# Kernel tuning notes

Hardware: AMD Instinct MI355X
Metric: run time of the kernel (lower is better)

Reference implementation:

```python
import jax, jax.numpy as jnp
import numpy as np

SCALE = 1.0  # module scale
# dropout is treated as identity (eval mode / deterministic reference)

def setup_inputs() -> dict:
    key = jax.random.key(0)
    k_x, k_w, k1, k2, k3 = jax.random.split(key, 5)
    B, S, D = 4, 4096, 1280
    x = jax.random.normal(k_x, (B, S, D), dtype=jnp.float32)
    W = jax.random.normal(k_w, (D, D), dtype=jnp.float32) * 0.02  # linear.weight [out, in]
    # kron factors are initialized to identity in the module; perturb slightly
    # so the rotation is non-trivial for correctness testing.
    kron_1 = jnp.eye(4, dtype=jnp.float32) + 0.01 * jax.random.normal(k1, (4, 4), dtype=jnp.float32)
    kron_2 = jnp.eye(8, dtype=jnp.float32) + 0.01 * jax.random.normal(k2, (8, 8), dtype=jnp.float32)
    kron_3 = jnp.eye(40, dtype=jnp.float32) + 0.01 * jax.random.normal(k3, (40, 40), dtype=jnp.float32)
    return {"x": x, "W": W, "kron_1": kron_1, "kron_2": kron_2, "kron_3": kron_3}

def reference(x, W, kron_1, kron_2, kron_3):
    # rotate_matrix = kron(kron(k1, k2), k3)  -> [in, in] = [1280, 1280]
    R = jnp.kron(jnp.kron(kron_1, kron_2), kron_3)
    # rotated_weight = (R @ W^T)^T ; F.linear(x, rotated_weight) = x @ (R @ W^T)
    rotated_weight = (R @ W.T).T  # [out, in]
    out = jnp.einsum('bsd,od->bso', x, rotated_weight)
    return out * SCALE
```

## Files before the change

kernel.cpp:

```cpp
#include <hip/hip_runtime.h>
#include <hip/hip_bf16.h>
#include <stdint.h>

typedef __bf16 bf16x8 __attribute__((ext_vector_type(8)));
typedef float floatx4 __attribute__((ext_vector_type(4)));

__device__ __forceinline__ void async_copy16(void* lds, const void* g) {
    __builtin_amdgcn_global_load_lds(
        (const __attribute__((address_space(1))) unsigned int*)g,
        (__attribute__((address_space(3))) unsigned int*)lds,
        16, 0, 0);
}

__global__ __launch_bounds__(256)
void prep(const float* __restrict__ x,
          const float* __restrict__ W,
          const float* __restrict__ K1,
          const float* __restrict__ K2,
          const float* __restrict__ K3,
          __hip_bfloat16* __restrict__ x_bf,
          __hip_bfloat16* __restrict__ Wrot,
          int nConv) {
    const int tid = threadIdx.x;

    if ((int)blockIdx.x < nConv) {
        const size_t i = ((size_t)blockIdx.x * 256 + tid) * 8;
        const float4 a = *(const float4*)(x + i);
        const float4 b = *(const float4*)(x + i + 4);
        bf16x8 v;
        v[0] = (__bf16)a.x; v[1] = (__bf16)a.y; v[2] = (__bf16)a.z; v[3] = (__bf16)a.w;
        v[4] = (__bf16)b.x; v[5] = (__bf16)b.y; v[6] = (__bf16)b.z; v[7] = (__bf16)b.w;
        *(bf16x8*)((__bf16*)x_bf + i) = v;
        return;
    }

    const int o = blockIdx.x - nConv;
    __shared__ __align__(16) float w0[1280];
    __shared__ __align__(16) float t1[1280];
    __shared__ __align__(16) float k3s[1600];
    __shared__ float k2s[64];
    __shared__ float k1s[16];

    for (int i = tid; i < 1280; i += 256) w0[i] = W[o * 1280 + i];
    for (int i = tid; i < 1600; i += 256) k3s[i] = K3[i];
    if (tid < 64) k2s[tid] = K2[tid];
    if (tid < 16) k1s[tid] = K1[tid];
    __syncthreads();

    for (int i = tid; i < 1280; i += 256) {
        const int p = i / 40, d3 = i % 40;
        const float4* w4 = (const float4*)(w0 + p * 40);
        const float4* k4 = (const float4*)(k3s + d3 * 40);
        float acc = 0.f;
#pragma unroll
        for (int t = 0; t < 10; ++t) {
            const float4 a = w4[t], b = k4[t];
            acc += a.x * b.x + a.y * b.y + a.z * b.z + a.w * b.w;
        }
        t1[i] = acc;
    }
    __syncthreads();

    for (int i = tid; i < 1280; i += 256) {
        const int d3 = i % 40, pd = i / 40;
        const int k1 = pd >> 3, d2 = pd & 7;
        float acc = 0.f;
#pragma unroll
        for (int k2 = 0; k2 < 8; ++k2) acc += t1[(k1 * 8 + k2) * 40 + d3] * k2s[d2 * 8 + k2];
        w0[i] = acc;
    }
    __syncthreads();

    for (int i = tid; i < 1280; i += 256) {
        const int d3 = i % 40, pd = i / 40;
        const int d1 = pd >> 3, d2 = pd & 7;
        float acc = 0.f;
#pragma unroll
        for (int k1 = 0; k1 < 4; ++k1) acc += w0[(k1 * 8 + d2) * 40 + d3] * k1s[d1 * 4 + k1];
        Wrot[(size_t)o * 1280 + i] = __float2bfloat16(acc);
    }
}

#define BM 128
#define BN 128
#define BK 64

__global__ __launch_bounds__(256)
void gemm_bt(const __hip_bfloat16* __restrict__ A,
             const __hip_bfloat16* __restrict__ B,
             float* __restrict__ C,
             int M, int N, int K) {
    __shared__ bf16x8 As[1024];
    __shared__ bf16x8 Bs[1024];

    const int tid  = threadIdx.x;
    const int wave = tid >> 6;
    const int lane = tid & 63;
    const int q    = lane >> 4;
    const int r16  = lane & 15;

    const int nTilesN = N / BN;
    const int nTilesM = M / BM;
    const int chunk   = nTilesM >> 3;
    const int xcd = blockIdx.x & 7;
    const int s   = blockIdx.x >> 3;
    const int bm  = xcd * chunk + s / nTilesN;
    const int bn  = s % nTilesN;
    const int tileM = bm * BM, tileN = bn * BN;
    const int wm = wave >> 1, wn = wave & 1;

    floatx4 acc[4][4];
#pragma unroll
    for (int i = 0; i < 4; ++i)
#pragma unroll
        for (int j = 0; j < 4; ++j) acc[i][j] = (floatx4){0.f, 0.f, 0.f, 0.f};

    for (int kt = 0; kt < K; kt += BK) {
#pragma unroll
        for (int t = 0; t < 4; ++t) {
            const int g  = wave * 256 + t * 64 + lane;
            const int m  = g >> 3;
            const int kv = (g & 7) ^ (m & 7);
            async_copy16(&As[wave * 256 + t * 64],
                         A + (size_t)(tileM + m) * K + kt + kv * 8);
            async_copy16(&Bs[wave * 256 + t * 64],
                         B + (size_t)(tileN + m) * K + kt + kv * 8);
        }
        __syncthreads();

#pragma unroll
        for (int s2 = 0; s2 < 2; ++s2) {
            bf16x8 af[4], bfr[4];
            const int kv = s2 * 4 + q;
#pragma unroll
            for (int i = 0; i < 4; ++i) {
                const int m = wm * 64 + i * 16 + r16;
                af[i] = As[m * 8 + (kv ^ (m & 7))];
                const int n = wn * 64 + i * 16 + r16;
                bfr[i] = Bs[n * 8 + (kv ^ (n & 7))];
            }
#pragma unroll
            for (int i = 0; i < 4; ++i)
#pragma unroll
                for (int j = 0; j < 4; ++j)
                    acc[i][j] = __builtin_amdgcn_mfma_f32_16x16x32_bf16(
                        af[i], bfr[j], acc[i][j], 0, 0, 0);
        }
        __syncthreads();
    }

#pragma unroll
    for (int i = 0; i < 4; ++i) {
#pragma unroll
        for (int j = 0; j < 4; ++j) {
            const int col = tileN + wn * 64 + j * 16 + r16;
#pragma unroll
            for (int r = 0; r < 4; ++r) {
                const int row = tileM + wm * 64 + i * 16 + q * 4 + r;
                C[(size_t)row * N + col] = acc[i][j][r];
            }
        }
    }
}

extern "C" void kernel_launch(void* const* d_in, const int* in_sizes, int n_in,
                              void* d_out, int out_size, void* d_ws, size_t ws_size,
                              hipStream_t stream) {
    const float* x  = (const float*)d_in[0];
    const float* W  = (const float*)d_in[1];
    const float* K1 = (const float*)d_in[2];
    const float* K2 = (const float*)d_in[3];
    const float* K3 = (const float*)d_in[4];
    float* out = (float*)d_out;

    const int D = 1280;
    const int M = in_sizes[0] / D;
    const int N = D, K = D;

    __hip_bfloat16* x_bf = (__hip_bfloat16*)d_ws;
    __hip_bfloat16* Wrot = x_bf + (size_t)M * K;

    const int nConv = (M * K) / (256 * 8);
    prep<<<nConv + D, 256, 0, stream>>>(x, W, K1, K2, K3, x_bf, Wrot, nConv);
    gemm_bt<<<(M / BM) * (N / BN), 256, 0, stream>>>(x_bf, Wrot, out, M, N, K);
}
```

Baseline: 240.1 us.

## Triple-buffer GEMM LDS tiles with async prefetch and a 256x128 block tile

The bf16 GEMM now uses a 256x128 output tile with 512 threads (8 waves). Global-to-LDS copies are triple-buffered, with tiles prefetched two k-steps ahead. Explicit vmcnt waits and raw barriers replace the per-step load-then-sync pattern, and the MFMA sections raise wave priority. The aim is to hide global load latency behind matrix math and cut barrier stalls. The cost is about 147KB of LDS per block, so only one block fits per CU despite the launch bound asking for two.

New measurement: 252.8 us. 5.3% more time.

```diff
diff --git a/kernel.cpp b/kernel.cpp
--- a/kernel.cpp
+++ b/kernel.cpp
@@ -81,17 +81,42 @@
     }
 }
 
-#define BM 128
+#define BM 256
 #define BN 128
 #define BK 64
-
-__global__ __launch_bounds__(256)
+#define AG (BM * BK / 8)
+#define BG (BN * BK / 8)
+
+__device__ __forceinline__ void stage_tile(const __hip_bfloat16* __restrict__ A,
+                                           const __hip_bfloat16* __restrict__ B,
+                                           bf16x8* Asb, bf16x8* Bsb,
+                                           int tileM, int tileN, int K, int kt,
+                                           int wave, int lane) {
+#pragma unroll
+    for (int c = 0; c < 4; ++c) {
+        const int g  = c * 512 + wave * 64 + lane;
+        const int m  = g >> 3;
+        const int kv = (g & 7) ^ (m & 7);
+        async_copy16(&Asb[c * 512 + wave * 64],
+                     A + (size_t)(tileM + m) * K + kt + kv * 8);
+    }
+#pragma unroll
+    for (int c = 0; c < 2; ++c) {
+        const int g  = c * 512 + wave * 64 + lane;
+        const int m  = g >> 3;
+        const int kv = (g & 7) ^ (m & 7);
+        async_copy16(&Bsb[c * 512 + wave * 64],
+                     B + (size_t)(tileN + m) * K + kt + kv * 8);
+    }
+}
+
+__global__ __launch_bounds__(512, 2)
 void gemm_bt(const __hip_bfloat16* __restrict__ A,
              const __hip_bfloat16* __restrict__ B,
              float* __restrict__ C,
              int M, int N, int K) {
-    __shared__ bf16x8 As[1024];
-    __shared__ bf16x8 Bs[1024];
+    __shared__ bf16x8 As[3 * AG];
+    __shared__ bf16x8 Bs[3 * BG];
 
     const int tid  = threadIdx.x;
     const int wave = tid >> 6;
@@ -115,19 +140,29 @@
 #pragma unroll
         for (int j = 0; j < 4; ++j) acc[i][j] = (floatx4){0.f, 0.f, 0.f, 0.f};
 
-    for (int kt = 0; kt < K; kt += BK) {
-#pragma unroll
-        for (int t = 0; t < 4; ++t) {
-            const int g  = wave * 256 + t * 64 + lane;
-            const int m  = g >> 3;
-            const int kv = (g & 7) ^ (m & 7);
-            async_copy16(&As[wave * 256 + t * 64],
-                         A + (size_t)(tileM + m) * K + kt + kv * 8);
-            async_copy16(&Bs[wave * 256 + t * 64],
-                         B + (size_t)(tileN + m) * K + kt + kv * 8);
-        }
-        __syncthreads();
-
+    const int nk = K / BK;
+
+    stage_tile(A, B, &As[0], &Bs[0], tileM, tileN, K, 0, wave, lane);
+    if (nk > 1)
+        stage_tile(A, B, &As[AG], &Bs[BG], tileM, tileN, K, BK, wave, lane);
+
+    int cur = 0;
+    for (int t = 0; t < nk; ++t) {
+        if (t + 2 < nk) {
+            const int nx = (cur >= 1) ? cur - 1 : cur + 2;
+            stage_tile(A, B, &As[nx * AG], &Bs[nx * BG],
+                       tileM, tileN, K, (t + 2) * BK, wave, lane);
+            asm volatile("s_waitcnt vmcnt(12)" ::: "memory");
+        } else if (t + 1 < nk) {
+            asm volatile("s_waitcnt vmcnt(6)" ::: "memory");
+        } else {
+            asm volatile("s_waitcnt vmcnt(0)" ::: "memory");
+        }
+        __builtin_amdgcn_s_barrier();
+        asm volatile("" ::: "memory");
+
+        const bf16x8* Ab = &As[cur * AG];
+        const bf16x8* Bb = &Bs[cur * BG];
 #pragma unroll
         for (int s2 = 0; s2 < 2; ++s2) {
             bf16x8 af[4], bfr[4];
@@ -135,18 +170,22 @@
 #pragma unroll
             for (int i = 0; i < 4; ++i) {
                 const int m = wm * 64 + i * 16 + r16;
-                af[i] = As[m * 8 + (kv ^ (m & 7))];
+                af[i] = Ab[m * 8 + (kv ^ (m & 7))];
                 const int n = wn * 64 + i * 16 + r16;
-                bfr[i] = Bs[n * 8 + (kv ^ (n & 7))];
+                bfr[i] = Bb[n * 8 + (kv ^ (n & 7))];
             }
+            __builtin_amdgcn_s_setprio(1);
 #pragma unroll
             for (int i = 0; i < 4; ++i)
 #pragma unroll
                 for (int j = 0; j < 4; ++j)
                     acc[i][j] = __builtin_amdgcn_mfma_f32_16x16x32_bf16(
                         af[i], bfr[j], acc[i][j], 0, 0, 0);
-        }
-        __syncthreads();
+            __builtin_amdgcn_s_setprio(0);
+        }
+        asm volatile("" ::: "memory");
+        __builtin_amdgcn_s_barrier();
+        cur = (cur == 2) ? 0 : cur + 1;
     }
 
 #pragma unroll
@@ -182,5 +221,5 @@
 
     const int nConv = (M * K) / (256 * 8);
     prep<<<nConv + D, 256, 0, stream>>>(x, W, K1, K2, K3, x_bf, Wrot, nConv);
-    gemm_bt<<<(M / BM) * (N / BN), 256, 0, stream>>>(x_bf, Wrot, out, M, N, K);
-}
+    gemm_bt<<<(M / BM) * (N / BN), 512, 0, stream>>>(x_bf, Wrot, out, M, N, K);
+}
```

## Restructure GEMM into 256x320 tiles with double-buffered LDS and interleaved prefetch

Applied to the files above, without the earlier changes.

The GEMM moves to 512-thread blocks computing 256x320 output tiles, so 1280 columns split into four N-tiles and the grid becomes 64x4 = 256 blocks. LDS is double-buffered, and the next K-slice's async global-to-LDS loads are spread across four MFMA phases with explicit waitcnt, barriers, sched_barrier and setprio, so copies overlap compute instead of stalling on a full sync each iteration. Larger tiles also raise operand reuse. The cost is 160 fp32 accumulators per thread and more LDS, which lowers occupancy. The hand-placed vmcnt values and block-wide barriers are fragile if the load counts change.

Result: faster. 219.1 us (-8.7%).

```diff
diff --git a/kernel.cpp b/kernel.cpp
--- a/kernel.cpp
+++ b/kernel.cpp
@@ -81,82 +81,190 @@
     }
 }
 
-#define BM 128
-#define BN 128
+#define BM 256
+#define BN 320
 #define BK 64
-
-__global__ __launch_bounds__(256)
+#define AGRAN 2048
+#define BGRAN 2560
+
+__global__ __launch_bounds__(512, 2)
 void gemm_bt(const __hip_bfloat16* __restrict__ A,
              const __hip_bfloat16* __restrict__ B,
              float* __restrict__ C,
              int M, int N, int K) {
-    __shared__ bf16x8 As[1024];
-    __shared__ bf16x8 Bs[1024];
+    __shared__ bf16x8 As[2][AGRAN];
+    __shared__ bf16x8 Bs[2][BGRAN];
 
     const int tid  = threadIdx.x;
     const int wave = tid >> 6;
     const int lane = tid & 63;
     const int q    = lane >> 4;
     const int r16  = lane & 15;
+    const int wm   = wave >> 2;
+    const int wn   = wave & 3;
 
     const int nTilesN = N / BN;
-    const int nTilesM = M / BM;
-    const int chunk   = nTilesM >> 3;
+    const int chunkM  = (M / BM) >> 3;
     const int xcd = blockIdx.x & 7;
     const int s   = blockIdx.x >> 3;
-    const int bm  = xcd * chunk + s / nTilesN;
+    const int bm  = xcd * chunkM + s / nTilesN;
     const int bn  = s % nTilesN;
     const int tileM = bm * BM, tileN = bn * BN;
-    const int wm = wave >> 1, wn = wave & 1;
-
-    floatx4 acc[4][4];
-#pragma unroll
-    for (int i = 0; i < 4; ++i)
-#pragma unroll
-        for (int j = 0; j < 4; ++j) acc[i][j] = (floatx4){0.f, 0.f, 0.f, 0.f};
-
-    for (int kt = 0; kt < K; kt += BK) {
-#pragma unroll
-        for (int t = 0; t < 4; ++t) {
-            const int g  = wave * 256 + t * 64 + lane;
-            const int m  = g >> 3;
-            const int kv = (g & 7) ^ (m & 7);
-            async_copy16(&As[wave * 256 + t * 64],
-                         A + (size_t)(tileM + m) * K + kt + kv * 8);
-            async_copy16(&Bs[wave * 256 + t * 64],
-                         B + (size_t)(tileN + m) * K + kt + kv * 8);
-        }
-        __syncthreads();
-
-#pragma unroll
-        for (int s2 = 0; s2 < 2; ++s2) {
-            bf16x8 af[4], bfr[4];
-            const int kv = s2 * 4 + q;
-#pragma unroll
-            for (int i = 0; i < 4; ++i) {
-                const int m = wm * 64 + i * 16 + r16;
-                af[i] = As[m * 8 + (kv ^ (m & 7))];
-                const int n = wn * 64 + i * 16 + r16;
-                bfr[i] = Bs[n * 8 + (kv ^ (n & 7))];
-            }
-#pragma unroll
-            for (int i = 0; i < 4; ++i)
-#pragma unroll
-                for (int j = 0; j < 4; ++j)
-                    acc[i][j] = __builtin_amdgcn_mfma_f32_16x16x32_bf16(
-                        af[i], bfr[j], acc[i][j], 0, 0, 0);
-        }
-        __syncthreads();
-    }
-
-#pragma unroll
-    for (int i = 0; i < 4; ++i) {
-#pragma unroll
-        for (int j = 0; j < 4; ++j) {
-            const int col = tileN + wn * 64 + j * 16 + r16;
+
+    uint32_t aoff[4], boff[5];
+#pragma unroll
+    for (int c = 0; c < 4; ++c) {
+        const int g = c * 512 + tid;
+        const int m = g >> 3, kv = (g & 7) ^ (m & 7);
+        aoff[c] = (uint32_t)(((tileM + m) * K + kv * 8) * 2);
+    }
+#pragma unroll
+    for (int c = 0; c < 5; ++c) {
+        const int g = c * 512 + tid;
+        const int m = g >> 3, kv = (g & 7) ^ (m & 7);
+        boff[c] = (uint32_t)(((tileN + m) * K + kv * 8) * 2);
+    }
+    const char* Abase = (const char*)A;
+    const char* Bbase = (const char*)B;
+
+    int ai[8], bi[5];
+#pragma unroll
+    for (int i = 0; i < 8; ++i) {
+        const int m = wm * 128 + i * 16 + r16;
+        ai[i] = m * 8 + (q ^ (m & 7));
+    }
+#pragma unroll
+    for (int j = 0; j < 5; ++j) {
+        const int n = wn * 80 + j * 16 + r16;
+        bi[j] = n * 8 + (q ^ (n & 7));
+    }
+
+    floatx4 acc[8][5];
+#pragma unroll
+    for (int i = 0; i < 8; ++i)
+#pragma unroll
+        for (int j = 0; j < 5; ++j) acc[i][j] = (floatx4){0.f, 0.f, 0.f, 0.f};
+
+    const int nk = K / BK;
+
+#pragma unroll
+    for (int c = 0; c < 4; ++c)
+        async_copy16(&As[0][c * 512 + wave * 64], Abase + aoff[c]);
+#pragma unroll
+    for (int c = 0; c < 5; ++c)
+        async_copy16(&Bs[0][c * 512 + wave * 64], Bbase + boff[c]);
+    asm volatile("s_waitcnt vmcnt(0)" ::: "memory");
+    __builtin_amdgcn_s_barrier();
+
+    bf16x8 bf0[5], bf1[5], af[4];
+
+    for (int t = 0; t < nk; ++t) {
+        const int cur = t & 1, nxt = cur ^ 1;
+        const uint32_t kb = (uint32_t)((t + 1) * BK * 2);
+        const bool hn = (t + 1 < nk);
+
+#pragma unroll
+        for (int i = 0; i < 4; ++i) af[i] = As[cur][ai[i]];
+#pragma unroll
+        for (int j = 0; j < 5; ++j) bf0[j] = Bs[cur][bi[j]];
+        if (hn) {
+            async_copy16(&As[nxt][0 * 512 + wave * 64], Abase + aoff[0] + kb);
+            async_copy16(&As[nxt][2 * 512 + wave * 64], Abase + aoff[2] + kb);
+            async_copy16(&Bs[nxt][0 * 512 + wave * 64], Bbase + boff[0] + kb);
+        }
+        __builtin_amdgcn_sched_barrier(0);
+        __builtin_amdgcn_s_barrier();
+        asm volatile("s_waitcnt lgkmcnt(0)" ::: "memory");
+        __builtin_amdgcn_sched_barrier(0);
+        __builtin_amdgcn_s_setprio(1);
+#pragma unroll
+        for (int i = 0; i < 4; ++i)
+#pragma unroll
+            for (int j = 0; j < 5; ++j)
+                acc[i][j] = __builtin_amdgcn_mfma_f32_16x16x32_bf16(
+                    af[i], bf0[j], acc[i][j], 0, 0, 0);
+        __builtin_amdgcn_s_setprio(0);
+        __builtin_amdgcn_sched_barrier(0);
+        __builtin_amdgcn_s_barrier();
+
+#pragma unroll
+        for (int i = 0; i < 4; ++i) af[i] = As[cur][ai[i] ^ 4];
+#pragma unroll
+        for (int j = 0; j < 5; ++j) bf1[j] = Bs[cur][bi[j] ^ 4];
+        if (hn) {
+            async_copy16(&Bs[nxt][1 * 512 + wave * 64], Bbase + boff[1] + kb);
+            async_copy16(&Bs[nxt][2 * 512 + wave * 64], Bbase + boff[2] + kb);
+            asm volatile("s_waitcnt vmcnt(5)" ::: "memory");
+        } else {
+            asm volatile("s_waitcnt vmcnt(0)" ::: "memory");
+        }
+        __builtin_amdgcn_sched_barrier(0);
+        __builtin_amdgcn_s_barrier();
+        asm volatile("s_waitcnt lgkmcnt(0)" ::: "memory");
+        __builtin_amdgcn_sched_barrier(0);
+        __builtin_amdgcn_s_setprio(1);
+#pragma unroll
+        for (int i = 0; i < 4; ++i)
+#pragma unroll
+            for (int j = 0; j < 5; ++j)
+                acc[i][j] = __builtin_amdgcn_mfma_f32_16x16x32_bf16(
+                    af[i], bf1[j], acc[i][j], 0, 0, 0);
+        __builtin_amdgcn_s_setprio(0);
+        __builtin_amdgcn_sched_barrier(0);
+        __builtin_amdgcn_s_barrier();
+
+#pragma unroll
+        for (int i = 0; i < 4; ++i) af[i] = As[cur][ai[4 + i]];
+        if (hn) {
+            async_copy16(&Bs[nxt][3 * 512 + wave * 64], Bbase + boff[3] + kb);
+            async_copy16(&Bs[nxt][4 * 512 + wave * 64], Bbase + boff[4] + kb);
+        }
+        __builtin_amdgcn_sched_barrier(0);
+        __builtin_amdgcn_s_barrier();
+        asm volatile("s_waitcnt lgkmcnt(0)" ::: "memory");
+        __builtin_amdgcn_sched_barrier(0);
+        __builtin_amdgcn_s_setprio(1);
+#pragma unroll
+        for (int i = 0; i < 4; ++i)
+#pragma unroll
+            for (int j = 0; j < 5; ++j)
+                acc[4 + i][j] = __builtin_amdgcn_mfma_f32_16x16x32_bf16(
+                    af[i], bf0[j], acc[4 + i][j], 0, 0, 0);
+        __builtin_amdgcn_s_setprio(0);
+        __builtin_amdgcn_sched_barrier(0);
+        __builtin_amdgcn_s_barrier();
+
+#pragma unroll
+        for (int i = 0; i < 4; ++i) af[i] = As[cur][ai[4 + i] ^ 4];
+        if (hn) {
+            async_copy16(&As[nxt][1 * 512 + wave * 64], Abase + aoff[1] + kb);
+            async_copy16(&As[nxt][3 * 512 + wave * 64], Abase + aoff[3] + kb);
+            asm volatile("s_waitcnt vmcnt(2)" ::: "memory");
+        }
+        __builtin_amdgcn_sched_barrier(0);
+        __builtin_amdgcn_s_barrier();
+        asm volatile("s_waitcnt lgkmcnt(0)" ::: "memory");
+        __builtin_amdgcn_sched_barrier(0);
+        __builtin_amdgcn_s_setprio(1);
+#pragma unroll
+        for (int i = 0; i < 4; ++i)
+#pragma unroll
+            for (int j = 0; j < 5; ++j)
+                acc[4 + i][j] = __builtin_amdgcn_mfma_f32_16x16x32_bf16(
+                    af[i], bf1[j], acc[4 + i][j], 0, 0, 0);
+        __builtin_amdgcn_s_setprio(0);
+        __builtin_amdgcn_sched_barrier(0);
+        __builtin_amdgcn_s_barrier();
+    }
+
+#pragma unroll
+    for (int i = 0; i < 8; ++i) {
+#pragma unroll
+        for (int j = 0; j < 5; ++j) {
+            const int col = tileN + wn * 80 + j * 16 + r16;
 #pragma unroll
             for (int r = 0; r < 4; ++r) {
-                const int row = tileM + wm * 64 + i * 16 + q * 4 + r;
+                const int row = tileM + wm * 128 + i * 16 + q * 4 + r;
                 C[(size_t)row * N + col] = acc[i][j][r];
             }
         }
@@ -182,5 +290,5 @@
 
     const int nConv = (M * K) / (256 * 8);
     prep<<<nConv + D, 256, 0, stream>>>(x, W, K1, K2, K3, x_bf, Wrot, nConv);
-    gemm_bt<<<(M / BM) * (N / BN), 256, 0, stream>>>(x_bf, Wrot, out, M, N, K);
-}
+    gemm_bt<<<(M / BM) * (N / BN), 512, 0, stream>>>(x_bf, Wrot, out, M, N, K);
+}
```
